# Optimization experiments

Hardware: AMD Instinct MI355X
Metric: run time of the kernel (lower is better)

## Reference

```python
import jax, jax.numpy as jnp
import numpy as np

N = 50000
E = 800000
D = 64


def _linear_params(key, d, bias=True):
    kw, kb = jax.random.split(key)
    s = 1.0 / np.sqrt(d)
    W = jax.random.uniform(kw, (d, d), jnp.float32, -s, s)
    if bias:
        b = jax.random.uniform(kb, (d,), jnp.float32, -s, s)
        return W, b
    return W


def setup_inputs() -> dict:
    key = jax.random.key(0)
    ks = jax.random.split(key, 12)
    x_src = jax.random.normal(ks[0], (N, D), jnp.float32)
    x_tgt = jax.random.normal(ks[1], (N, D), jnp.float32)
    t_src = jax.random.normal(ks[2], (N, D), jnp.float32)
    t_tgt = jax.random.normal(ks[3], (N, D), jnp.float32)
    edge_index = jax.random.randint(ks[4], (2, E), 0, N, jnp.int64)
    W_x = _linear_params(ks[5], D, bias=False)
    W_t = _linear_params(ks[6], D, bias=False)
    Ka_W, Ka_b = _linear_params(ks[7], D)
    Qa_W, Qa_b = _linear_params(ks[8], D)
    Kb_W, Kb_b = _linear_params(ks[9], D)
    Qb_W, Qb_b = _linear_params(ks[10], D)
    return dict(x_src=x_src, x_tgt=x_tgt, t_src=t_src, t_tgt=t_tgt,
                edge_index=edge_index, W_x=W_x, W_t=W_t,
                Ka_W=Ka_W, Ka_b=Ka_b, Qa_W=Qa_W, Qa_b=Qa_b,
                Kb_W=Kb_W, Kb_b=Kb_b, Qb_W=Qb_W, Qb_b=Qb_b)


def _segment_softmax(scores, seg, num_segments):
    # numerically stable softmax over edges sharing the same destination node
    m = jax.ops.segment_max(scores, seg, num_segments=num_segments)
    ex = jnp.exp(scores - m[seg])
    denom = jax.ops.segment_sum(ex, seg, num_segments=num_segments)
    return ex / denom[seg]


def reference(x_src, x_tgt, t_src, t_tgt, edge_index,
              W_x, W_t, Ka_W, Ka_b, Qa_W, Qa_b, Kb_W, Kb_b, Qb_W, Qb_b):
    row, col = edge_index[0], edge_index[1]
    n = x_tgt.shape[0]
    d = x_src.shape[-1]
    scale = 1.0 / jnp.sqrt(jnp.float32(d))

    # project on nodes first (cheaper than per-edge), then gather per edge
    q_alpha = (t_tgt @ Qa_W.T + Qa_b)[row]   # [E, D]
    k_alpha = (t_src @ Ka_W.T + Ka_b)[col]
    alpha = _segment_softmax(jnp.sum(q_alpha * k_alpha, -1) * scale, row, n)

    q_beta = (x_tgt @ Qb_W.T + Qb_b)[row]
    k_beta = (x_src @ Kb_W.T + Kb_b)[col]
    beta = _segment_softmax(jnp.sum(q_beta * k_beta, -1) * scale, row, n)

    msg_t = alpha[:, None] * (t_src @ W_t.T)[col]  # [E, D]
    msg_x = beta[:, None] * (x_src @ W_x.T)[col]

    out_x = jax.ops.segment_sum(msg_x, row, num_segments=n)
    out_t = jax.ops.segment_sum(msg_t, row, num_segments=n)
    return out_x, out_t
```

## Files before the change

### kernel.cpp

```cpp
#include <hip/hip_runtime.h>
#include <math.h>


#define D 64
#define NINF -3.0e38f
typedef unsigned short ushortT;
typedef unsigned long long ull;
typedef __attribute__((ext_vector_type(8))) short bf16x8;
typedef __attribute__((ext_vector_type(4))) float f32x4;

__device__ __forceinline__ float b2f_lo(unsigned u) {
  return __uint_as_float(u << 16);
}
__device__ __forceinline__ float b2f_hi(unsigned u) {
  return __uint_as_float(u & 0xffff0000u);
}
__device__ __forceinline__ ushortT f2b(float f) {
  unsigned u = __float_as_uint(f);
  u += 0x7fffu + ((u >> 16) & 1u);
  return (ushortT)(u >> 16);
}
__device__ __forceinline__ bf16x8 pack8(float4 v0, float4 v1) {
  bf16x8 r;
  r[0] = (short)f2b(v0.x); r[1] = (short)f2b(v0.y);
  r[2] = (short)f2b(v0.z); r[3] = (short)f2b(v0.w);
  r[4] = (short)f2b(v1.x); r[5] = (short)f2b(v1.y);
  r[6] = (short)f2b(v1.z); r[7] = (short)f2b(v1.w);
  return r;
}

__device__ __forceinline__ bool wave_is64(const ull* __restrict__ ei, ull nNodes) {
  ull v = ei[threadIdx.x & 63];
  return __ballot(v >= nNodes) == 0ull;
}

__global__ __launch_bounds__(256) void scat(
    const void* __restrict__ ei, int* __restrict__ deg,
    int* __restrict__ ecol, int CAP, int E, int N) {
  const bool is64 = wave_is64((const ull*)ei, (ull)N);
  const int gid = blockIdx.x * 256 + threadIdx.x;
  const int base = gid << 3;
  if (base >= E) return;
  const int m = (E - base) < 8 ? (E - base) : 8;

  int r[8], c[8], rk[8];
  if (is64) {
    const long long* p = (const long long*)ei;
    if (m == 8) {
#pragma unroll
      for (int j = 0; j < 8; ++j) {
        r[j] = (int)p[base + j];
        c[j] = (int)p[(long long)E + base + j];
      }
#pragma unroll
      for (int j = 0; j < 8; ++j) rk[j] = atomicAdd(&deg[r[j]], 1);
#pragma unroll
      for (int j = 0; j < 8; ++j)
        if (rk[j] < CAP) ecol[(size_t)r[j] * CAP + rk[j]] = c[j];
    } else {
      for (int j = 0; j < m; ++j) {
        int rr = (int)p[base + j];
        int cc = (int)p[(long long)E + base + j];
        int k = atomicAdd(&deg[rr], 1);
        if (k < CAP) ecol[(size_t)rr * CAP + k] = cc;
      }
    }
  } else {
    const int* p = (const int*)ei;
    if (m == 8) {
#pragma unroll
      for (int j = 0; j < 8; ++j) {
        r[j] = p[base + j];
        c[j] = p[E + base + j];
      }
#pragma unroll
      for (int j = 0; j < 8; ++j) rk[j] = atomicAdd(&deg[r[j]], 1);
#pragma unroll
      for (int j = 0; j < 8; ++j)
        if (rk[j] < CAP) ecol[(size_t)r[j] * CAP + rk[j]] = c[j];
    } else {
      for (int j = 0; j < m; ++j) {
        int rr = p[base + j];
        int cc = p[E + base + j];
        int k = atomicAdd(&deg[rr], 1);
        if (k < CAP) ecol[(size_t)rr * CAP + k] = cc;
      }
    }
  }
}

__global__ __launch_bounds__(256) void proj(
    const float* __restrict__ t_tgt, const float* __restrict__ x_tgt,
    const float* __restrict__ t_src, const float* __restrict__ x_src,
    const float* __restrict__ QaW, const float* __restrict__ Qab_,
    const float* __restrict__ QbW, const float* __restrict__ Qbb,
    const float* __restrict__ KaW, const float* __restrict__ Kab_,
    const float* __restrict__ Wt,
    const float* __restrict__ KbW, const float* __restrict__ Kbb,
    const float* __restrict__ Wx,
    float* __restrict__ qab, ushortT* __restrict__ kab, ushortT* __restrict__ vtx,
    int N, int bpj) {
  const int tid = threadIdx.x;
  const int tile = blockIdx.x;
  const int job = tile / bpj;
  const int jb = tile % bpj;
  const float *X, *W0, *B0, *W1 = nullptr;
  switch (job) {
    case 0: X = t_tgt; W0 = QaW; B0 = Qab_; break;
    case 1: X = x_tgt; W0 = QbW; B0 = Qbb; break;
    case 2: X = t_src; W0 = KaW; B0 = Kab_; W1 = Wt; break;
    default: X = x_src; W0 = KbW; B0 = Kbb; W1 = Wx; break;
  }
  const bool dual = (job >= 2);
  const int half = (job & 1) ? 64 : 0;
  const int base = jb * 128;

  const int lane = tid & 63;
  const int wid = tid >> 6;
  const int m16 = lane & 15;
  const int quad = lane >> 4;

  f32x4 acc0[2][4], acc1[2][4];
#pragma unroll
  for (int mt = 0; mt < 2; ++mt)
#pragma unroll
    for (int nt = 0; nt < 4; ++nt) {
      acc0[mt][nt] = (f32x4){0.f, 0.f, 0.f, 0.f};
      acc1[mt][nt] = (f32x4){0.f, 0.f, 0.f, 0.f};
    }

#pragma unroll
  for (int ko = 0; ko < 2; ++ko) {
    const int koff = ko * 32 + quad * 8;
    bf16x8 a[2];
#pragma unroll
    for (int mt = 0; mt < 2; ++mt) {
      const int gnode = base + wid * 32 + mt * 16 + m16;
      float4 v0 = make_float4(0.f, 0.f, 0.f, 0.f), v1 = v0;
      if (gnode < N) {
        const float* p = X + (size_t)gnode * D + koff;
        v0 = *(const float4*)p;
        v1 = *(const float4*)(p + 4);
      }
      a[mt] = pack8(v0, v1);
    }
#pragma unroll
    for (int nt = 0; nt < 4; ++nt) {
      const float* pw = W0 + (nt * 16 + m16) * D + koff;
      bf16x8 b = pack8(*(const float4*)pw, *(const float4*)(pw + 4));
#pragma unroll
      for (int mt = 0; mt < 2; ++mt)
        acc0[mt][nt] = __builtin_amdgcn_mfma_f32_16x16x32_bf16(
            a[mt], b, acc0[mt][nt], 0, 0, 0);
    }
    if (dual) {
#pragma unroll
      for (int nt = 0; nt < 4; ++nt) {
        const float* pw = W1 + (nt * 16 + m16) * D + koff;
        bf16x8 b = pack8(*(const float4*)pw, *(const float4*)(pw + 4));
#pragma unroll
        for (int mt = 0; mt < 2; ++mt)
          acc1[mt][nt] = __builtin_amdgcn_mfma_f32_16x16x32_bf16(
              a[mt], b, acc1[mt][nt], 0, 0, 0);
      }
    }
  }

  float bias[4];
#pragma unroll
  for (int nt = 0; nt < 4; ++nt) bias[nt] = B0[nt * 16 + m16];
#pragma unroll
  for (int mt = 0; mt < 2; ++mt) {
#pragma unroll
    for (int reg = 0; reg < 4; ++reg) {
      int node = base + wid * 32 + mt * 16 + quad * 4 + reg;
      if (node < N) {
        if (!dual) {
          float* dst = qab + (size_t)node * 128 + half;
#pragma unroll
          for (int nt = 0; nt < 4; ++nt)
            dst[nt * 16 + m16] = acc0[mt][nt][reg] + bias[nt];
        } else {
          ushortT* dk = kab + (size_t)node * 128 + half;
          ushortT* dv = vtx + (size_t)node * 128 + half;
#pragma unroll
          for (int nt = 0; nt < 4; ++nt) {
            dk[nt * 16 + m16] = f2b(acc0[mt][nt][reg] + bias[nt]);
            dv[nt * 16 + m16] = f2b(acc1[mt][nt][reg]);
          }
        }
      }
    }
  }
}

__global__ __launch_bounds__(256) void node_attn(
    const float* __restrict__ qab, const ushortT* __restrict__ kab,
    const ushortT* __restrict__ vtx,
    const int* __restrict__ deg, const int* __restrict__ ecol, int CAP,
    float* __restrict__ out_x, float* __restrict__ out_t, int nNodes) {
  const int lane = threadIdx.x & 63;
  const int sub = lane >> 4;
  const int sl = lane & 15;
  const int gw = (blockIdx.x * blockDim.x + threadIdx.x) >> 6;
  const int nw = (gridDim.x * blockDim.x) >> 6;
  const float scale = 0.125f;

  for (int n = gw; n < nNodes; n += nw) {
    int dg = deg[n];
    if (dg > CAP) dg = CAP;
    const size_t nb = (size_t)n * D;
    if (dg == 0) {
      out_t[nb + lane] = 0.f;
      out_x[nb + lane] = 0.f;
      continue;
    }
    const size_t s = (size_t)n * CAP;
    const float4 q0 = *(const float4*)(qab + (size_t)n * 128 + sl * 8);
    const float4 q1 = *(const float4*)(qab + (size_t)n * 128 + sl * 8 + 4);

    float m = NINF, d = 0.f;
    float acc[8];
#pragma unroll
    for (int j = 0; j < 8; ++j) acc[j] = 0.f;

    for (int i = 0; i < dg; i += 8) {
      const int i0 = i + sub;
      const int i1 = i + 4 + sub;
      const bool a0 = i0 < dg, a1 = i1 < dg;
      const int c0 = ecol[s + (a0 ? i0 : 0)];
      const int c1 = ecol[s + (a1 ? i1 : 0)];
      const uint4 k0 = *(const uint4*)(kab + (size_t)c0 * 128 + sl * 8);
      const uint4 v0 = *(const uint4*)(vtx + (size_t)c0 * 128 + sl * 8);
      const uint4 k1 = *(const uint4*)(kab + (size_t)c1 * 128 + sl * 8);
      const uint4 v1 = *(const uint4*)(vtx + (size_t)c1 * 128 + sl * 8);

      {
        float t = q0.x * b2f_lo(k0.x);
        t = fmaf(q0.y, b2f_hi(k0.x), t);
        t = fmaf(q0.z, b2f_lo(k0.y), t);
        t = fmaf(q0.w, b2f_hi(k0.y), t);
        t = fmaf(q1.x, b2f_lo(k0.z), t);
        t = fmaf(q1.y, b2f_hi(k0.z), t);
        t = fmaf(q1.z, b2f_lo(k0.w), t);
        t = fmaf(q1.w, b2f_hi(k0.w), t);
#pragma unroll
        for (int off = 1; off < 8; off <<= 1) t += __shfl_xor(t, off);
        const float sc = a0 ? t * scale : NINF;
        const float mN = fmaxf(m, sc);
        const float f = __expf(m - mN);
        const float w = a0 ? __expf(sc - mN) : 0.f;
        d = d * f + w;
        acc[0] = fmaf(acc[0], f, w * b2f_lo(v0.x));
        acc[1] = fmaf(acc[1], f, w * b2f_hi(v0.x));
        acc[2] = fmaf(acc[2], f, w * b2f_lo(v0.y));
        acc[3] = fmaf(acc[3], f, w * b2f_hi(v0.y));
        acc[4] = fmaf(acc[4], f, w * b2f_lo(v0.z));
        acc[5] = fmaf(acc[5], f, w * b2f_hi(v0.z));
        acc[6] = fmaf(acc[6], f, w * b2f_lo(v0.w));
        acc[7] = fmaf(acc[7], f, w * b2f_hi(v0.w));
        m = mN;
      }
      {
        float t = q0.x * b2f_lo(k1.x);
        t = fmaf(q0.y, b2f_hi(k1.x), t);
        t = fmaf(q0.z, b2f_lo(k1.y), t);
        t = fmaf(q0.w, b2f_hi(k1.y), t);
        t = fmaf(q1.x, b2f_lo(k1.z), t);
        t = fmaf(q1.y, b2f_hi(k1.z), t);
        t = fmaf(q1.z, b2f_lo(k1.w), t);
        t = fmaf(q1.w, b2f_hi(k1.w), t);
#pragma unroll
        for (int off = 1; off < 8; off <<= 1) t += __shfl_xor(t, off);
        const float sc = a1 ? t * scale : NINF;
        const float mN = fmaxf(m, sc);
        const float f = __expf(m - mN);
        const float w = a1 ? __expf(sc - mN) : 0.f;
        d = d * f + w;
        acc[0] = fmaf(acc[0], f, w * b2f_lo(v1.x));
        acc[1] = fmaf(acc[1], f, w * b2f_hi(v1.x));
        acc[2] = fmaf(acc[2], f, w * b2f_lo(v1.y));
        acc[3] = fmaf(acc[3], f, w * b2f_hi(v1.y));
        acc[4] = fmaf(acc[4], f, w * b2f_lo(v1.z));
        acc[5] = fmaf(acc[5], f, w * b2f_hi(v1.z));
        acc[6] = fmaf(acc[6], f, w * b2f_lo(v1.w));
        acc[7] = fmaf(acc[7], f, w * b2f_hi(v1.w));
        m = mN;
      }
    }

    float mg = m;
#pragma unroll
    for (int off = 16; off < 64; off <<= 1) mg = fmaxf(mg, __shfl_xor(mg, off));
    const float fg = __expf(m - mg);
    d *= fg;
#pragma unroll
    for (int j = 0; j < 8; ++j) acc[j] *= fg;
#pragma unroll
    for (int off = 16; off < 64; off <<= 1) {
      d += __shfl_xor(d, off);
#pragma unroll
      for (int j = 0; j < 8; ++j) acc[j] += __shfl_xor(acc[j], off);
    }
    const float inv = 1.0f / d;
    if (sub == 0) {
      float4 o0, o1;
      o0.x = acc[0] * inv; o0.y = acc[1] * inv;
      o0.z = acc[2] * inv; o0.w = acc[3] * inv;
      o1.x = acc[4] * inv; o1.y = acc[5] * inv;
      o1.z = acc[6] * inv; o1.w = acc[7] * inv;
      float* dst = (sl < 8) ? (out_t + nb + sl * 8) : (out_x + nb + (sl - 8) * 8);
      *(float4*)dst = o0;
      *(float4*)(dst + 4) = o1;
    }
  }
}

extern "C" void kernel_launch(void* const* d_in, const int* in_sizes, int n_in,
                              void* d_out, int out_size, void* d_ws, size_t ws_size,
                              hipStream_t stream) {
  const float* x_src = (const float*)d_in[0];
  const float* x_tgt = (const float*)d_in[1];
  const float* t_src = (const float*)d_in[2];
  const float* t_tgt = (const float*)d_in[3];
  const void* edge_index = d_in[4];
  const float* W_x = (const float*)d_in[5];
  const float* W_t = (const float*)d_in[6];
  const float* Ka_W = (const float*)d_in[7];
  const float* Ka_b = (const float*)d_in[8];
  const float* Qa_W = (const float*)d_in[9];
  const float* Qa_b = (const float*)d_in[10];
  const float* Kb_W = (const float*)d_in[11];
  const float* Kb_b = (const float*)d_in[12];
  const float* Qb_W = (const float*)d_in[13];
  const float* Qb_b = (const float*)d_in[14];

  const int N = in_sizes[0] / D;
  const int E = in_sizes[4] / 2;

  char* ws = (char*)d_ws;
  size_t ofs = 0;
  auto carve = [&](size_t bytes) {
    size_t p = ofs;
    ofs += (bytes + 255) & ~(size_t)255;
    return p;
  };
  float* qab = (float*)(ws + carve((size_t)N * 128 * 4));
  ushortT* kab = (ushortT*)(ws + carve((size_t)N * 128 * 2));
  ushortT* vtx = (ushortT*)(ws + carve((size_t)N * 128 * 2));
  int* deg = (int*)(ws + carve((size_t)N * 4));
  size_t avail = (ws_size > ofs) ? (ws_size - ofs) : 0;
  int CAP = (int)(avail / ((size_t)N * 4));
  if (CAP > 128) CAP = 128;
  if (CAP < 64) CAP = 64;
  int* ecol = (int*)(ws + carve((size_t)N * CAP * 4));

  float* out_x = (float*)d_out;
  float* out_t = out_x + (size_t)N * D;

  const int scatGrid = (E + 8 * 256 - 1) / (8 * 256);
  const int bpj = (N + 127) / 128;

  hipMemsetAsync(deg, 0, (size_t)N * 4, stream);
  scat<<<scatGrid, 256, 0, stream>>>(edge_index, deg, ecol, CAP, E, N);
  proj<<<4 * bpj, 256, 0, stream>>>(
      t_tgt, x_tgt, t_src, x_src,
      Qa_W, Qa_b, Qb_W, Qb_b,
      Ka_W, Ka_b, W_t,
      Kb_W, Kb_b, W_x,
      qab, kab, vtx, N, bpj);
  node_attn<<<(N + 3) / 4, 256, 0, stream>>>(qab, kab, vtx, deg, ecol, CAP,
                                             out_x, out_t, N);
}
```

Measured before the change: 249.3 us.

## Build compact CSR via two-pass radix bucketing instead of atomic fixed-capacity adjacency

Replaces the global-atomic scatter into a per-node fixed-capacity column table with a radix-style CSR build. Edges are packed as 16-bit row and column values, histogrammed by the high row byte, scattered into buckets, then sorted per bucket in shared memory to produce offsets and 16-bit column indices. The goal is to remove contended global atomics, the large sparse ecol buffer and the degree cap, while giving node_attn compact contiguous neighbour lists. In exchange it adds three extra launches and a serial single-block scan, and it assumes N fits in 16 bits and that each bucket holds at most 8192 edges.

Result: slower. 291.4 us (+16.9%).

```diff
diff --git a/kernel.cpp b/kernel.cpp
--- a/kernel.cpp
+++ b/kernel.cpp
@@ -4,6 +4,7 @@
 
 #define D 64
 #define NINF -3.0e38f
+#define CHUNK 4096
 typedef unsigned short ushortT;
 typedef unsigned long long ull;
 typedef __attribute__((ext_vector_type(8))) short bf16x8;
@@ -34,59 +35,133 @@
   return __ballot(v >= nNodes) == 0ull;
 }
 
-__global__ __launch_bounds__(256) void scat(
-    const void* __restrict__ ei, int* __restrict__ deg,
-    int* __restrict__ ecol, int CAP, int E, int N) {
+__global__ __launch_bounds__(256) void pack_hist(
+    const void* __restrict__ ei, unsigned* __restrict__ packed,
+    int* __restrict__ hist, int E, int N) {
+  __shared__ int h[256];
+  const int t = threadIdx.x;
+  h[t] = 0;
+  __syncthreads();
   const bool is64 = wave_is64((const ull*)ei, (ull)N);
-  const int gid = blockIdx.x * 256 + threadIdx.x;
-  const int base = gid << 3;
-  if (base >= E) return;
-  const int m = (E - base) < 8 ? (E - base) : 8;
-
-  int r[8], c[8], rk[8];
+  const int base = blockIdx.x * CHUNK + t;
   if (is64) {
     const long long* p = (const long long*)ei;
-    if (m == 8) {
-#pragma unroll
-      for (int j = 0; j < 8; ++j) {
-        r[j] = (int)p[base + j];
-        c[j] = (int)p[(long long)E + base + j];
-      }
-#pragma unroll
-      for (int j = 0; j < 8; ++j) rk[j] = atomicAdd(&deg[r[j]], 1);
-#pragma unroll
-      for (int j = 0; j < 8; ++j)
-        if (rk[j] < CAP) ecol[(size_t)r[j] * CAP + rk[j]] = c[j];
-    } else {
-      for (int j = 0; j < m; ++j) {
-        int rr = (int)p[base + j];
-        int cc = (int)p[(long long)E + base + j];
-        int k = atomicAdd(&deg[rr], 1);
-        if (k < CAP) ecol[(size_t)rr * CAP + k] = cc;
+#pragma unroll 4
+    for (int k = 0; k < 16; ++k) {
+      int e = base + k * 256;
+      if (e < E) {
+        unsigned r = (unsigned)(int)p[e];
+        unsigned c = (unsigned)(int)p[(long long)E + e];
+        packed[e] = (r << 16) | c;
+        atomicAdd(&h[r >> 8], 1);
       }
     }
   } else {
     const int* p = (const int*)ei;
-    if (m == 8) {
-#pragma unroll
-      for (int j = 0; j < 8; ++j) {
-        r[j] = p[base + j];
-        c[j] = p[E + base + j];
-      }
-#pragma unroll
-      for (int j = 0; j < 8; ++j) rk[j] = atomicAdd(&deg[r[j]], 1);
-#pragma unroll
-      for (int j = 0; j < 8; ++j)
-        if (rk[j] < CAP) ecol[(size_t)r[j] * CAP + rk[j]] = c[j];
-    } else {
-      for (int j = 0; j < m; ++j) {
-        int rr = p[base + j];
-        int cc = p[E + base + j];
-        int k = atomicAdd(&deg[rr], 1);
-        if (k < CAP) ecol[(size_t)rr * CAP + k] = cc;
-      }
-    }
-  }
+#pragma unroll 4
+    for (int k = 0; k < 16; ++k) {
+      int e = base + k * 256;
+      if (e < E) {
+        unsigned r = (unsigned)p[e];
+        unsigned c = (unsigned)p[E + e];
+        packed[e] = (r << 16) | c;
+        atomicAdd(&h[r >> 8], 1);
+      }
+    }
+  }
+  __syncthreads();
+  hist[blockIdx.x * 256 + t] = h[t];
+}
+
+__global__ __launch_bounds__(256) void scan_hist(
+    int* __restrict__ hist, int* __restrict__ bucketStart,
+    int* __restrict__ offs, int nBlocks, int E, int N) {
+  __shared__ int tot[256], sc[256];
+  const int t = threadIdx.x;
+  int p = 0;
+  for (int b = 0; b < nBlocks; ++b) {
+    int v = hist[b * 256 + t];
+    hist[b * 256 + t] = p;
+    p += v;
+  }
+  tot[t] = p;
+  sc[t] = p;
+  __syncthreads();
+  for (int off = 1; off < 256; off <<= 1) {
+    int add = (t >= off) ? sc[t - off] : 0;
+    __syncthreads();
+    sc[t] += add;
+    __syncthreads();
+  }
+  const int binbase = sc[t] - tot[t];
+  for (int b = 0; b < nBlocks; ++b) hist[b * 256 + t] += binbase;
+  bucketStart[t] = binbase;
+  if (t == 0) {
+    bucketStart[256] = E;
+    offs[N] = E;
+  }
+}
+
+__global__ __launch_bounds__(256) void scatter_bucket(
+    const unsigned* __restrict__ packed, const int* __restrict__ hist,
+    unsigned* __restrict__ bucketed, int E) {
+  __shared__ int baseA[256];
+  __shared__ int cnt[256];
+  const int t = threadIdx.x;
+  baseA[t] = hist[blockIdx.x * 256 + t];
+  cnt[t] = 0;
+  __syncthreads();
+  const int base = blockIdx.x * CHUNK + t;
+#pragma unroll 4
+  for (int k = 0; k < 16; ++k) {
+    int e = base + k * 256;
+    if (e < E) {
+      unsigned v = packed[e];
+      int bin = v >> 24;
+      int dst = baseA[bin] + atomicAdd(&cnt[bin], 1);
+      bucketed[dst] = v;
+    }
+  }
+}
+
+__global__ __launch_bounds__(256) void build_csr(
+    const unsigned* __restrict__ bucketed, const int* __restrict__ bucketStart,
+    int* __restrict__ offs, ushortT* __restrict__ ecol, int N) {
+  __shared__ int cnt[256], sc[256], cnt2[256];
+  __shared__ ushortT lcol[8192];
+  const int t = threadIdx.x;
+  const int b = blockIdx.x;
+  const int start = bucketStart[b];
+  int nb = bucketStart[b + 1] - start;
+  if (nb > 8192) nb = 8192;
+  cnt[t] = 0;
+  cnt2[t] = 0;
+  __syncthreads();
+  for (int i = t; i < nb; i += 256)
+    atomicAdd(&cnt[(bucketed[start + i] >> 16) & 255], 1);
+  __syncthreads();
+  const int c = cnt[t];
+  sc[t] = c;
+  __syncthreads();
+  for (int off = 1; off < 256; off <<= 1) {
+    int add = (t >= off) ? sc[t - off] : 0;
+    __syncthreads();
+    sc[t] += add;
+    __syncthreads();
+  }
+  const int loffs_t = sc[t] - c;
+  sc[t] = loffs_t;
+  const int row = b * 256 + t;
+  if (row < N) offs[row] = start + loffs_t;
+  __syncthreads();
+  for (int i = t; i < nb; i += 256) {
+    unsigned v = bucketed[start + i];
+    int r = (v >> 16) & 255;
+    int pos = sc[r] + atomicAdd(&cnt2[r], 1);
+    lcol[pos] = (ushortT)(v & 0xFFFFu);
+  }
+  __syncthreads();
+  for (int i = t; i < nb; i += 256) ecol[start + i] = lcol[i];
 }
 
 __global__ __launch_bounds__(256) void proj(
@@ -147,21 +222,21 @@
 #pragma unroll
     for (int nt = 0; nt < 4; ++nt) {
       const float* pw = W0 + (nt * 16 + m16) * D + koff;
-      bf16x8 b = pack8(*(const float4*)pw, *(const float4*)(pw + 4));
+      bf16x8 bfr = pack8(*(const float4*)pw, *(const float4*)(pw + 4));
 #pragma unroll
       for (int mt = 0; mt < 2; ++mt)
         acc0[mt][nt] = __builtin_amdgcn_mfma_f32_16x16x32_bf16(
-            a[mt], b, acc0[mt][nt], 0, 0, 0);
+            a[mt], bfr, acc0[mt][nt], 0, 0, 0);
     }
     if (dual) {
 #pragma unroll
       for (int nt = 0; nt < 4; ++nt) {
         const float* pw = W1 + (nt * 16 + m16) * D + koff;
-        bf16x8 b = pack8(*(const float4*)pw, *(const float4*)(pw + 4));
+        bf16x8 bfr = pack8(*(const float4*)pw, *(const float4*)(pw + 4));
 #pragma unroll
         for (int mt = 0; mt < 2; ++mt)
           acc1[mt][nt] = __builtin_amdgcn_mfma_f32_16x16x32_bf16(
-              a[mt], b, acc1[mt][nt], 0, 0, 0);
+              a[mt], bfr, acc1[mt][nt], 0, 0, 0);
       }
     }
   }
@@ -197,7 +272,7 @@
 __global__ __launch_bounds__(256) void node_attn(
     const float* __restrict__ qab, const ushortT* __restrict__ kab,
     const ushortT* __restrict__ vtx,
-    const int* __restrict__ deg, const int* __restrict__ ecol, int CAP,
+    const int* __restrict__ offs, const ushortT* __restrict__ ecol,
     float* __restrict__ out_x, float* __restrict__ out_t, int nNodes) {
   const int lane = threadIdx.x & 63;
   const int sub = lane >> 4;
@@ -207,15 +282,14 @@
   const float scale = 0.125f;
 
   for (int n = gw; n < nNodes; n += nw) {
-    int dg = deg[n];
-    if (dg > CAP) dg = CAP;
+    const int s = offs[n];
+    const int dg = offs[n + 1] - s;
     const size_t nb = (size_t)n * D;
     if (dg == 0) {
       out_t[nb + lane] = 0.f;
       out_x[nb + lane] = 0.f;
       continue;
     }
-    const size_t s = (size_t)n * CAP;
     const float4 q0 = *(const float4*)(qab + (size_t)n * 128 + sl * 8);
     const float4 q1 = *(const float4*)(qab + (size_t)n * 128 + sl * 8 + 4);
 
@@ -228,8 +302,8 @@
       const int i0 = i + sub;
       const int i1 = i + 4 + sub;
       const bool a0 = i0 < dg, a1 = i1 < dg;
-      const int c0 = ecol[s + (a0 ? i0 : 0)];
-      const int c1 = ecol[s + (a1 ? i1 : 0)];
+      const int c0 = (int)ecol[s + (a0 ? i0 : 0)];
+      const int c1 = (int)ecol[s + (a1 ? i1 : 0)];
       const uint4 k0 = *(const uint4*)(kab + (size_t)c0 * 128 + sl * 8);
       const uint4 v0 = *(const uint4*)(vtx + (size_t)c0 * 128 + sl * 8);
       const uint4 k1 = *(const uint4*)(kab + (size_t)c1 * 128 + sl * 8);
@@ -348,27 +422,30 @@
   float* qab = (float*)(ws + carve((size_t)N * 128 * 4));
   ushortT* kab = (ushortT*)(ws + carve((size_t)N * 128 * 2));
   ushortT* vtx = (ushortT*)(ws + carve((size_t)N * 128 * 2));
-  int* deg = (int*)(ws + carve((size_t)N * 4));
-  size_t avail = (ws_size > ofs) ? (ws_size - ofs) : 0;
-  int CAP = (int)(avail / ((size_t)N * 4));
-  if (CAP > 128) CAP = 128;
-  if (CAP < 64) CAP = 64;
-  int* ecol = (int*)(ws + carve((size_t)N * CAP * 4));
+  unsigned* packed = (unsigned*)(ws + carve((size_t)E * 4));
+  unsigned* bucketed = (unsigned*)(ws + carve((size_t)E * 4));
+  ushortT* ecol = (ushortT*)(ws + carve((size_t)E * 2));
+  const int nBlocks = (E + CHUNK - 1) / CHUNK;
+  int* hist = (int*)(ws + carve((size_t)nBlocks * 256 * 4));
+  int* bucketStart = (int*)(ws + carve(257 * 4));
+  int* offs = (int*)(ws + carve(((size_t)N + 1) * 4));
+  (void)ws_size;
 
   float* out_x = (float*)d_out;
   float* out_t = out_x + (size_t)N * D;
 
-  const int scatGrid = (E + 8 * 256 - 1) / (8 * 256);
   const int bpj = (N + 127) / 128;
 
-  hipMemsetAsync(deg, 0, (size_t)N * 4, stream);
-  scat<<<scatGrid, 256, 0, stream>>>(edge_index, deg, ecol, CAP, E, N);
+  pack_hist<<<nBlocks, 256, 0, stream>>>(edge_index, packed, hist, E, N);
+  scan_hist<<<1, 256, 0, stream>>>(hist, bucketStart, offs, nBlocks, E, N);
+  scatter_bucket<<<nBlocks, 256, 0, stream>>>(packed, hist, bucketed, E);
+  build_csr<<<256, 256, 0, stream>>>(bucketed, bucketStart, offs, ecol, N);
   proj<<<4 * bpj, 256, 0, stream>>>(
       t_tgt, x_tgt, t_src, x_src,
       Qa_W, Qa_b, Qb_W, Qb_b,
       Ka_W, Ka_b, W_t,
       Kb_W, Kb_b, W_x,
       qab, kab, vtx, N, bpj);
-  node_attn<<<(N + 3) / 4, 256, 0, stream>>>(qab, kab, vtx, deg, ecol, CAP,
+  node_attn<<<(N + 3) / 4, 256, 0, stream>>>(qab, kab, vtx, offs, ecol,
                                              out_x, out_t, N);
 }
```
